# Kernel optimization log

Hardware: AMD Instinct MI355X
Metric: run time of the kernel (lower is better)

The kernel has to match this reference:

```python
import jax, jax.numpy as jnp
import numpy as np

EPS = 1e-12  # matches torch F.normalize default eps

def _l2norm(x, axis):
    n = jnp.sqrt(jnp.sum(x * x, axis=axis, keepdims=True))
    return x / jnp.maximum(n, EPS)

def setup_inputs() -> dict:
    key = jax.random.key(0)
    k1, k2, k3 = jax.random.split(key, 3)
    bs, V, N = 2, 4096, 32
    S, K = 8, 64
    neighbor_index = jax.random.randint(k1, (bs, V, N), 0, V)
    vertices = jax.random.normal(k2, (bs, V, 3), dtype=jnp.float32)
    directions = jax.random.normal(k3, (3, S * K), dtype=jnp.float32) * (1.0 / np.sqrt(S * K))
    return {"neighbor_index": neighbor_index, "vertices": vertices, "directions": directions}

def reference(neighbor_index, vertices, directions):
    # neighbor_index: (bs, V, N) int; vertices: (bs, V, 3); directions: (3, S*K)
    bs, V, N = neighbor_index.shape
    S, K = 8, 64
    id0 = jnp.arange(bs)[:, None, None]
    neighbors = vertices[id0, neighbor_index]                    # (bs, V, N, 3) gather
    nd = _l2norm(neighbors - vertices[:, :, None, :], axis=-1)   # (bs, V, N, 3)
    sd = _l2norm(directions, axis=0)                             # (3, S*K)
    theta = jax.nn.relu(jnp.einsum('bvnd,dm->bvnm', nd, sd))     # (bs, V, N, S*K)
    theta = theta.reshape(bs, V, N, S, K)
    theta = jnp.max(theta, axis=2)                               # max over neighbors
    feature = jnp.sum(theta, axis=2)                             # sum over supports -> (bs, V, K)
    return feature
```

## Files before the change

### kernel.cpp

```cpp
#include <hip/hip_runtime.h>

#define BS 2
#define V_DIM 4096
#define N_NBR 32
#define S_SUP 8
#define K_OUT 64
#define SK (S_SUP * K_OUT)
#define WAVES_PER_BLOCK 4
#define EPS 1e-12f

typedef float f32x2 __attribute__((ext_vector_type(2)));

__global__ __launch_bounds__(WAVES_PER_BLOCK * 64) void conv_surface_kernel(
    const int* __restrict__ nidx,
    const float* __restrict__ verts,
    const float* __restrict__ dirs,
    float* __restrict__ out)
{
    const int lane = threadIdx.x & 63;
    const int wave = threadIdx.x >> 6;
    const int vi   = blockIdx.x * WAVES_PER_BLOCK + wave;
    const int b    = vi / V_DIM;
    const int bbase = b * V_DIM;

    __shared__ float snd[WAVES_PER_BLOCK][3][N_NBR];

    float a0[S_SUP], a1[S_SUP], a2[S_SUP];
#pragma unroll
    for (int s = 0; s < S_SUP; ++s) {
        const int m = s * K_OUT + lane;
        a0[s] = dirs[0 * SK + m];
        a1[s] = dirs[1 * SK + m];
        a2[s] = dirs[2 * SK + m];
    }

    const float cx = verts[vi * 3 + 0];
    const float cy = verts[vi * 3 + 1];
    const float cz = verts[vi * 3 + 2];

    if (lane < N_NBR) {
        const int j = nidx[vi * N_NBR + lane];
        const float dx = verts[(bbase + j) * 3 + 0] - cx;
        const float dy = verts[(bbase + j) * 3 + 1] - cy;
        const float dz = verts[(bbase + j) * 3 + 2] - cz;
        const float inv = 1.0f / fmaxf(sqrtf(dx * dx + dy * dy + dz * dz), EPS);
        snd[wave][0][lane] = dx * inv;
        snd[wave][1][lane] = dy * inv;
        snd[wave][2][lane] = dz * inv;
    }

    f32x2 D0[S_SUP / 2], D1[S_SUP / 2], D2[S_SUP / 2];
#pragma unroll
    for (int j = 0; j < S_SUP / 2; ++j) {
        const int s0 = 2 * j, s1 = 2 * j + 1;
        const float i0 = 1.0f / fmaxf(sqrtf(a0[s0] * a0[s0] + a1[s0] * a1[s0] + a2[s0] * a2[s0]), EPS);
        const float i1 = 1.0f / fmaxf(sqrtf(a0[s1] * a0[s1] + a1[s1] * a1[s1] + a2[s1] * a2[s1]), EPS);
        D0[j] = (f32x2){a0[s0] * i0, a0[s1] * i1};
        D1[j] = (f32x2){a1[s0] * i0, a1[s1] * i1};
        D2[j] = (f32x2){a2[s0] * i0, a2[s1] * i1};
    }

    __syncthreads();

    f32x2 th[S_SUP / 2];
#pragma unroll
    for (int j = 0; j < S_SUP / 2; ++j) th[j] = (f32x2){0.0f, 0.0f};

#pragma unroll
    for (int n = 0; n < N_NBR; ++n) {
        const float nx = snd[wave][0][n];
        const float ny = snd[wave][1][n];
        const float nz = snd[wave][2][n];
        const f32x2 vx = (f32x2){nx, nx};
        const f32x2 vy = (f32x2){ny, ny};
        const f32x2 vz = (f32x2){nz, nz};
#pragma unroll
        for (int j = 0; j < S_SUP / 2; ++j) {
            f32x2 t = vx * D0[j];
            t = t + vy * D1[j];
            t = t + vz * D2[j];
            th[j] = __builtin_elementwise_max(th[j], t);
        }
    }

    float acc = 0.0f;
#pragma unroll
    for (int j = 0; j < S_SUP / 2; ++j) acc += th[j].x + th[j].y;

    out[vi * K_OUT + lane] = acc;
}

extern "C" void kernel_launch(void* const* d_in, const int* in_sizes, int n_in,
                              void* d_out, int out_size, void* d_ws, size_t ws_size,
                              hipStream_t stream) {
    const int*   nidx  = (const int*)d_in[0];
    const float* verts = (const float*)d_in[1];
    const float* dirs  = (const float*)d_in[2];
    float*       out   = (float*)d_out;

    const int total_v = BS * V_DIM;
    const int blocks  = total_v / WAVES_PER_BLOCK;
    conv_surface_kernel<<<blocks, WAVES_PER_BLOCK * 64, 0, stream>>>(nidx, verts, dirs, out);
}
```

Before: 18.21 us.

## Process two vertices per wave with readlane broadcast instead of LDS

Each wave now handles two vertices: the lower half of the lanes gathers and normalizes the 32 neighbor directions for one vertex and the upper half does the same for the other. The per-neighbor values are broadcast to all lanes with readlane, which removes the shared-memory staging and the block barrier. The block grows to 1024 threads and each wave loads and normalizes the direction table once for two vertices. The cost is half as many waves, so there is less parallelism on a kernel that is already small, plus scalar readlane overhead inside the inner loop.

```diff
diff --git a/kernel.cpp b/kernel.cpp
--- a/kernel.cpp
+++ b/kernel.cpp
@@ -6,12 +6,19 @@
 #define S_SUP 8
 #define K_OUT 64
 #define SK (S_SUP * K_OUT)
-#define WAVES_PER_BLOCK 4
 #define EPS 1e-12f
+
+#define BLOCK_THREADS 1024
+#define WAVES_PER_BLOCK (BLOCK_THREADS / 64)
+#define VERTS_PER_WAVE 2
 
 typedef float f32x2 __attribute__((ext_vector_type(2)));
 
-__global__ __launch_bounds__(WAVES_PER_BLOCK * 64) void conv_surface_kernel(
+__device__ __forceinline__ float bcast(float x, int srclane) {
+    return __uint_as_float(__builtin_amdgcn_readlane(__float_as_uint(x), (unsigned)srclane));
+}
+
+__global__ __launch_bounds__(BLOCK_THREADS, 4) void conv_surface_kernel(
     const int* __restrict__ nidx,
     const float* __restrict__ verts,
     const float* __restrict__ dirs,
@@ -19,11 +26,8 @@
 {
     const int lane = threadIdx.x & 63;
     const int wave = threadIdx.x >> 6;
-    const int vi   = blockIdx.x * WAVES_PER_BLOCK + wave;
-    const int b    = vi / V_DIM;
-    const int bbase = b * V_DIM;
-
-    __shared__ float snd[WAVES_PER_BLOCK][3][N_NBR];
+    const int gw   = blockIdx.x * WAVES_PER_BLOCK + wave;
+    const int v0   = gw * VERTS_PER_WAVE;
 
     float a0[S_SUP], a1[S_SUP], a2[S_SUP];
 #pragma unroll
@@ -34,60 +38,69 @@
         a2[s] = dirs[2 * SK + m];
     }
 
-    const float cx = verts[vi * 3 + 0];
-    const float cy = verts[vi * 3 + 1];
-    const float cz = verts[vi * 3 + 2];
+    const int h  = lane >> 5;
+    const int ln = lane & 31;
+    const int vg = v0 + h;
+    const int bbase = (vg >> 12) << 12;
 
-    if (lane < N_NBR) {
-        const int j = nidx[vi * N_NBR + lane];
-        const float dx = verts[(bbase + j) * 3 + 0] - cx;
-        const float dy = verts[(bbase + j) * 3 + 1] - cy;
-        const float dz = verts[(bbase + j) * 3 + 2] - cz;
-        const float inv = 1.0f / fmaxf(sqrtf(dx * dx + dy * dy + dz * dz), EPS);
-        snd[wave][0][lane] = dx * inv;
-        snd[wave][1][lane] = dy * inv;
-        snd[wave][2][lane] = dz * inv;
-    }
+    const int j  = nidx[vg * N_NBR + ln];
+    const float cx = verts[vg * 3 + 0];
+    const float cy = verts[vg * 3 + 1];
+    const float cz = verts[vg * 3 + 2];
+
+    const float gx = verts[(bbase + j) * 3 + 0];
+    const float gy = verts[(bbase + j) * 3 + 1];
+    const float gz = verts[(bbase + j) * 3 + 2];
 
     f32x2 D0[S_SUP / 2], D1[S_SUP / 2], D2[S_SUP / 2];
 #pragma unroll
-    for (int j = 0; j < S_SUP / 2; ++j) {
-        const int s0 = 2 * j, s1 = 2 * j + 1;
-        const float i0 = 1.0f / fmaxf(sqrtf(a0[s0] * a0[s0] + a1[s0] * a1[s0] + a2[s0] * a2[s0]), EPS);
-        const float i1 = 1.0f / fmaxf(sqrtf(a0[s1] * a0[s1] + a1[s1] * a1[s1] + a2[s1] * a2[s1]), EPS);
-        D0[j] = (f32x2){a0[s0] * i0, a0[s1] * i1};
-        D1[j] = (f32x2){a1[s0] * i0, a1[s1] * i1};
-        D2[j] = (f32x2){a2[s0] * i0, a2[s1] * i1};
+    for (int p = 0; p < S_SUP / 2; ++p) {
+        const int s0 = 2 * p, s1 = 2 * p + 1;
+        const float i0 = 1.0f / fmaxf(sqrtf(a0[s0]*a0[s0] + a1[s0]*a1[s0] + a2[s0]*a2[s0]), EPS);
+        const float i1 = 1.0f / fmaxf(sqrtf(a0[s1]*a0[s1] + a1[s1]*a1[s1] + a2[s1]*a2[s1]), EPS);
+        D0[p] = (f32x2){a0[s0] * i0, a0[s1] * i1};
+        D1[p] = (f32x2){a1[s0] * i0, a1[s1] * i1};
+        D2[p] = (f32x2){a2[s0] * i0, a2[s1] * i1};
     }
 
-    __syncthreads();
-
-    f32x2 th[S_SUP / 2];
-#pragma unroll
-    for (int j = 0; j < S_SUP / 2; ++j) th[j] = (f32x2){0.0f, 0.0f};
+    const float dx = gx - cx;
+    const float dy = gy - cy;
+    const float dz = gz - cz;
+    const float inv = 1.0f / fmaxf(sqrtf(dx*dx + dy*dy + dz*dz), EPS);
+    const float ndx = dx * inv;
+    const float ndy = dy * inv;
+    const float ndz = dz * inv;
 
 #pragma unroll
-    for (int n = 0; n < N_NBR; ++n) {
-        const float nx = snd[wave][0][n];
-        const float ny = snd[wave][1][n];
-        const float nz = snd[wave][2][n];
-        const f32x2 vx = (f32x2){nx, nx};
-        const f32x2 vy = (f32x2){ny, ny};
-        const f32x2 vz = (f32x2){nz, nz};
+    for (int v = 0; v < VERTS_PER_WAVE; ++v) {
+        f32x2 th[S_SUP / 2];
 #pragma unroll
-        for (int j = 0; j < S_SUP / 2; ++j) {
-            f32x2 t = vx * D0[j];
-            t = t + vy * D1[j];
-            t = t + vz * D2[j];
-            th[j] = __builtin_elementwise_max(th[j], t);
+        for (int p = 0; p < S_SUP / 2; ++p) th[p] = (f32x2){0.0f, 0.0f};
+
+        const int base = v * 32;
+#pragma unroll 8
+        for (int n = 0; n < N_NBR; ++n) {
+            const float nx = bcast(ndx, base + n);
+            const float ny = bcast(ndy, base + n);
+            const float nz = bcast(ndz, base + n);
+            const f32x2 vx = (f32x2){nx, nx};
+            const f32x2 vy = (f32x2){ny, ny};
+            const f32x2 vz = (f32x2){nz, nz};
+#pragma unroll
+            for (int p = 0; p < S_SUP / 2; ++p) {
+                f32x2 t = vx * D0[p];
+                t = t + vy * D1[p];
+                t = t + vz * D2[p];
+                th[p] = __builtin_elementwise_max(th[p], t);
+            }
         }
+
+        float acc = 0.0f;
+#pragma unroll
+        for (int p = 0; p < S_SUP / 2; ++p) acc += th[p].x + th[p].y;
+
+        out[(v0 + v) * K_OUT + lane] = acc;
     }
-
-    float acc = 0.0f;
-#pragma unroll
-    for (int j = 0; j < S_SUP / 2; ++j) acc += th[j].x + th[j].y;
-
-    out[vi * K_OUT + lane] = acc;
 }
 
 extern "C" void kernel_launch(void* const* d_in, const int* in_sizes, int n_in,
@@ -99,6 +112,6 @@
     float*       out   = (float*)d_out;
 
     const int total_v = BS * V_DIM;
-    const int blocks  = total_v / WAVES_PER_BLOCK;
-    conv_surface_kernel<<<blocks, WAVES_PER_BLOCK * 64, 0, stream>>>(nidx, verts, dirs, out);
+    const int blocks  = total_v / (WAVES_PER_BLOCK * VERTS_PER_WAVE);
+    conv_surface_kernel<<<blocks, BLOCK_THREADS, 0, stream>>>(nidx, verts, dirs, out);
 }
```

Measured after the change: 19.10 us. 4.8% more time.
